# Optimization experiments

Measured on AMD Instinct MI355X. Metric: run time of the kernel, lower is better.

## Reference

```python
import jax, jax.numpy as jnp
import numpy as np

B, N, D = 8, 8192, 512
WS = 128          # ATTENTION_WINDOW_SIZE
LB = 1            # ATTENTION_WINDOW_LOOKBACK (look_backward)
NW = N // WS      # number of windows (N divisible by WS -> autopad no-op)


def setup_inputs() -> dict:
    key = jax.random.key(0)
    ks = jax.random.split(key, 4)
    s = 0.02
    return {
        "x": jax.random.normal(ks[0], (B, N, D), dtype=jnp.float32),
        "w_q": jax.random.normal(ks[1], (D, D), dtype=jnp.float32) * s,
        "b_q": jnp.zeros((D,), dtype=jnp.float32),
        "w_k": jax.random.normal(ks[2], (D, D), dtype=jnp.float32) * s,
        "b_k": jnp.zeros((D,), dtype=jnp.float32),
        "w_v": jax.random.normal(ks[3], (D, D), dtype=jnp.float32) * s,
        "b_v": jnp.zeros((D,), dtype=jnp.float32),
    }


def _look_around(t, pad_value):
    # t: (B, NW, WS, ...) -> concat of [backward..current] windows along window-length axis
    pad_width = [(0, 0), (LB, 0)] + [(0, 0)] * (t.ndim - 2)
    padded = jnp.pad(t, pad_width, constant_values=pad_value)
    return jnp.concatenate([padded[:, i:i + NW] for i in range(LB + 1)], axis=2)


def _local_attention(q, k, v):
    scale = D ** -0.5
    bq = q.reshape(B, NW, WS, D)
    bk = _look_around(k.reshape(B, NW, WS, D), 0.0)   # (B, NW, (LB+1)*WS, D)
    bv = _look_around(v.reshape(B, NW, WS, D), 0.0)

    # absolute position ticks for causal + padding masks
    tq = jnp.arange(N).reshape(1, NW, WS)                               # query positions
    tk = _look_around(jnp.arange(N).reshape(1, NW, WS), -1)             # key positions, -1 = pad

    sim = jnp.einsum('bwie,bwje->bwij', bq, bk) * scale                 # (B, NW, WS, (LB+1)*WS)
    mask = (tq[..., :, None] < tk[..., None, :]) | (tk[..., None, :] < 0)
    sim = jnp.where(mask, -jnp.finfo(sim.dtype).max, sim)
    attn = jax.nn.softmax(sim, axis=-1)                                  # dropout = 0 -> no-op
    out = jnp.einsum('bwij,bwje->bwie', attn, bv)
    return out.reshape(B, N, D)


def reference(x, w_q, b_q, w_k, b_k, w_v, b_v):
    q = x @ w_q.T + b_q
    k = x @ w_k.T + b_k
    v = x @ w_v.T + b_v
    return _local_attention(q, k, v)
```

## Files before the change

### kernel.cpp

```cpp
#include <hip/hip_runtime.h>


typedef __bf16 bf16x8 __attribute__((ext_vector_type(8)));
typedef float f32x4 __attribute__((ext_vector_type(4)));
typedef unsigned short u16x8 __attribute__((ext_vector_type(8)));

#define BATCH 8
#define SEQ   8192
#define DIM   512
#define NWIN  64
#define TOKS  (BATCH * SEQ)
#define WSELEM ((size_t)TOKS * DIM)

__device__ __forceinline__ unsigned short f2b(float f) {
    union { float f; unsigned int u; } c; c.f = f;
    unsigned int u = c.u;
    return (unsigned short)((u + 0x7FFFu + ((u >> 16) & 1u)) >> 16);
}

__device__ __forceinline__ int swz64(int row, int col) {
    return (row * 64 + col) ^ ((row & 7) << 3);
}

__device__ __forceinline__ void gload_lds16(const unsigned short* g,
                                            unsigned short* l) {
    __builtin_amdgcn_global_load_lds(
        (const __attribute__((address_space(1))) void*)g,
        (__attribute__((address_space(3))) void*)l, 16, 0, 0);
}

__global__ __launch_bounds__(256) void k_cvt(const float* __restrict__ s,
                                             unsigned short* __restrict__ d,
                                             int n8) {
    const int stride = gridDim.x * blockDim.x;
    for (int i = blockIdx.x * blockDim.x + threadIdx.x; i < n8; i += stride) {
        const float4 a = ((const float4*)s)[2 * i];
        const float4 b = ((const float4*)s)[2 * i + 1];
        u16x8 v;
        v[0] = f2b(a.x); v[1] = f2b(a.y); v[2] = f2b(a.z); v[3] = f2b(a.w);
        v[4] = f2b(b.x); v[5] = f2b(b.y); v[6] = f2b(b.z); v[7] = f2b(b.w);
        ((u16x8*)d)[i] = v;
    }
}

__global__ __launch_bounds__(256, 2) void k_qkv(
    const unsigned short* __restrict__ xb, const unsigned short* __restrict__ wb,
    const float* __restrict__ bq, const float* __restrict__ bk,
    const float* __restrict__ bv,
    unsigned short* __restrict__ qo, unsigned short* __restrict__ ko,
    unsigned short* __restrict__ vto)
{
    __shared__ __align__(16) unsigned short sm[32768];
    unsigned short* Xs = sm;

    int bid = (int)blockIdx.x;
    bid = (bid & 7) * 256 + (bid >> 3);
    const int mt = bid >> 2, nt = bid & 3;
    const int rbase = mt << 7;
    const int cbase = nt << 7;

    const unsigned short* __restrict__ xsrc0 = xb + ((size_t)rbase << 9);
    const unsigned short* __restrict__ wsrc0 = wb + ((size_t)cbase << 9);

    const int tid  = threadIdx.x;
    const int lane = tid & 63;
    const int wid  = tid >> 6;
    const int wm = wid >> 1, wn = wid & 1;
    const int l15 = lane & 15, lg = lane >> 4;

    f32x4 acc[3][4][4];
#pragma unroll
    for (int s = 0; s < 3; ++s)
#pragma unroll
        for (int m = 0; m < 4; ++m)
#pragma unroll
            for (int n = 0; n < 4; ++n) acc[s][m][n] = (f32x4){0.f, 0.f, 0.f, 0.f};

    const int srow = tid >> 3;
    const int gs   = ((tid & 7) ^ (srow & 7)) << 3;
    const int ldso = tid << 3;

    for (int ks = 0; ks < 8; ++ks) {
        const int kc = ks << 6;
#pragma unroll
        for (int i = 0; i < 4; ++i) {
            const int row = (i << 5) + srow;
            gload_lds16(xsrc0 + ((size_t)row << 9) + kc + gs, Xs + (i << 11) + ldso);
        }
#pragma unroll
        for (int ws = 0; ws < 3; ++ws) {
#pragma unroll
            for (int i = 0; i < 4; ++i) {
                const int row = (i << 5) + srow;
                gload_lds16(wsrc0 + ((size_t)ws << 18) + ((size_t)row << 9) + kc + gs,
                            sm + 8192 + (ws << 13) + (i << 11) + ldso);
            }
        }
        __syncthreads();
#pragma unroll
        for (int kk = 0; kk < 64; kk += 32) {
            const int cu = kk + (lg << 3);
            bf16x8 af[4];
#pragma unroll
            for (int m = 0; m < 4; ++m)
                af[m] = *(const bf16x8*)&Xs[swz64((wm << 6) + (m << 4) + l15, cu)];
#pragma unroll
            for (int ws = 0; ws < 3; ++ws) {
                const unsigned short* Wsb = sm + 8192 + (ws << 13);
                bf16x8 bfr[4];
#pragma unroll
                for (int n = 0; n < 4; ++n)
                    bfr[n] = *(const bf16x8*)&Wsb[swz64((wn << 6) + (n << 4) + l15, cu)];
#pragma unroll
                for (int m = 0; m < 4; ++m)
#pragma unroll
                    for (int n = 0; n < 4; ++n)
                        acc[ws][m][n] = __builtin_amdgcn_mfma_f32_16x16x32_bf16(
                            af[m], bfr[n], acc[ws][m][n], 0, 0, 0);
            }
        }
        __syncthreads();
    }

#pragma unroll
    for (int ws = 0; ws < 2; ++ws) {
        unsigned short* __restrict__ out = ws ? ko : qo;
        const float* __restrict__ bias = ws ? bk : bq;
#pragma unroll
        for (int n = 0; n < 4; ++n) {
            const int col = cbase + (wn << 6) + (n << 4) + l15;
            const float bv_ = bias[col];
#pragma unroll
            for (int m = 0; m < 4; ++m)
#pragma unroll
                for (int j = 0; j < 4; ++j) {
                    const int row = rbase + (wm << 6) + (m << 4) + (lg << 2) + j;
                    out[(size_t)row * DIM + col] = f2b(acc[ws][m][n][j] + bv_);
                }
        }
    }
#pragma unroll
    for (int n = 0; n < 4; ++n) {
        const int dv = (wn << 6) + (n << 4) + l15;
        const float bv_ = bv[cbase + dv];
#pragma unroll
        for (int m = 0; m < 4; ++m)
#pragma unroll
            for (int j = 0; j < 4; ++j) {
                const int tok = (wm << 6) + (m << 4) + (lg << 2) + j;
                sm[tok * 129 + dv] = f2b(acc[2][m][n][j] + bv_);
            }
    }
    __syncthreads();
    {
        const int batch = rbase >> 13;
        const int c5_0  = (rbase & 8191) >> 5;
#pragma unroll
        for (int s = 0; s < 8; ++s) {
            const int c5sel = s & 3, dvh = s >> 2;
            const int dvl  = (dvh << 6) + (wid << 4) + (lane >> 2);
            const int keyo = (lane & 3) << 3;
            const int tok0 = (c5sel << 5) + keyo;
            u16x8 v;
#pragma unroll
            for (int j = 0; j < 8; ++j) v[j] = sm[(tok0 + j) * 129 + dvl];
            *(u16x8*)&vto[((size_t)((batch * 256 + c5_0 + c5sel) * 512
                                    + cbase + dvl) << 5) + keyo] = v;
        }
    }
}

__global__ __launch_bounds__(512, 2) void k_attn(
    const unsigned short* __restrict__ q,
    const unsigned short* __restrict__ k,
    const unsigned short* __restrict__ vt3,
    float* __restrict__ out)
{
    __shared__ __align__(16) unsigned short Kb[32768];
    __shared__ __align__(16) unsigned short Pl[32768];

    int bid = (int)blockIdx.x;
    bid = (bid & 7) * 64 + (bid >> 3);
    const int b = bid >> 6, w = bid & 63;
    const int tid  = threadIdx.x;
    const int lane = tid & 63, wid = tid >> 6;
    const int l15 = lane & 15, lg = lane >> 4;
    const int kstart = (w - 1) << 7;
    const size_t qrow0 = ((size_t)b << 13) + ((size_t)w << 7);
    const size_t kbase = (size_t)b << 13;

    const int srow = tid >> 3;
    const int s0   = tid & 7;

    f32x4 acc[16];
#pragma unroll
    for (int n = 0; n < 16; ++n) acc[n] = (f32x4){0.f, 0.f, 0.f, 0.f};

    auto stageK = [&](int buf, int ds) {
#pragma unroll
        for (int i = 0; i < 4; ++i) {
            const int r = (i << 6) + srow;
            int krow = kstart + r; krow = krow < 0 ? 0 : krow;
            gload_lds16(k + (kbase + krow) * DIM + (ds << 6) + ((s0 ^ (r & 7)) << 3),
                        Kb + (buf << 14) + (i << 12) + (tid << 3));
        }
    };

    stageK(0, 0);
    stageK(1, 1);
    __syncthreads();
    for (int ds = 0; ds < 8; ++ds) {
        const unsigned short* Kc = Kb + ((ds & 1) << 14);
#pragma unroll
        for (int kk2 = 0; kk2 < 2; ++kk2) {
            const int cu = (kk2 << 5) + (lg << 3);
            const bf16x8 af = *(const bf16x8*)
                &q[(qrow0 + (wid << 4) + l15) * DIM + (ds << 6) + cu];
#pragma unroll
            for (int n = 0; n < 16; ++n) {
                const bf16x8 bf = *(const bf16x8*)&Kc[swz64((n << 4) + l15, cu)];
                acc[n] = __builtin_amdgcn_mfma_f32_16x16x32_bf16(af, bf, acc[n], 0, 0, 0);
            }
        }
        __syncthreads();
        if (ds + 2 < 8) stageK(ds & 1, ds + 2);
    }

    const int c5base = kstart >> 5;
    auto stageV = [&](int buf, int kk) {
        int c5 = c5base + kk; c5 = c5 < 0 ? 0 : c5;
        const unsigned short* src = vt3 + ((size_t)(b * 256 + c5) << 14);
#pragma unroll
        for (int i = 0; i < 4; ++i)
            gload_lds16(src + (i << 12) + (tid << 3),
                        Kb + (buf << 14) + (i << 12) + (tid << 3));
    };
    stageV(0, 0);
    stageV(1, 1);

    const float scale = 0.04419417382415922f;
    float inv[4];
    unsigned short* Pw = Pl + (wid << 12);
#pragma unroll
    for (int jj = 0; jj < 4; ++jj) {
        const int r  = (lg << 2) + jj;
        const int qr = (wid << 4) + r;
        float mx = -3.0e38f;
#pragma unroll
        for (int n = 0; n < 16; ++n) {
            const int c = (n << 4) + l15;
            const bool keep = (c <= qr + 128) && (w > 0 || c >= 128);
            const float s = keep ? acc[n][jj] * scale : -INFINITY;
            acc[n][jj] = s;
            mx = fmaxf(mx, s);
        }
#pragma unroll
        for (int o = 1; o < 16; o <<= 1) mx = fmaxf(mx, __shfl_xor(mx, o));
        float sum = 0.f;
#pragma unroll
        for (int n = 0; n < 16; ++n) {
            const float p = __expf(acc[n][jj] - mx);
            acc[n][jj] = p;
            sum += p;
        }
#pragma unroll
        for (int o = 1; o < 16; o <<= 1) sum += __shfl_xor(sum, o);
        inv[jj] = 1.0f / sum;
#pragma unroll
        for (int n = 0; n < 16; ++n) {
            const int c = (n << 4) + l15;
            Pw[(r << 8) + ((((c >> 3) ^ r) << 3) | (c & 7))] = f2b(acc[n][jj]);
        }
    }
    __syncthreads();

    f32x4 oacc[32];
#pragma unroll
    for (int n = 0; n < 32; ++n) oacc[n] = (f32x4){0.f, 0.f, 0.f, 0.f};

    for (int kk = 0; kk < 8; ++kk) {
        const unsigned short* Vc = Kb + ((kk & 1) << 14);
        const bf16x8 pa = *(const bf16x8*)
            &Pw[(l15 << 8) + ((((kk << 2) + lg) ^ l15) << 3)];
#pragma unroll
        for (int n = 0; n < 32; ++n) {
            const bf16x8 bv_ = *(const bf16x8*)&Vc[(((n << 4) + l15) << 5) + (lg << 3)];
            oacc[n] = __builtin_amdgcn_mfma_f32_16x16x32_bf16(pa, bv_, oacc[n], 0, 0, 0);
        }
        if (kk < 7) {
            __syncthreads();
            if (kk + 2 < 8) stageV(kk & 1, kk + 2);
        }
    }

#pragma unroll
    for (int n = 0; n < 32; ++n) {
        const int dv = (n << 4) + l15;
        float* orow = out + (qrow0 + (wid << 4) + (lg << 2)) * DIM + dv;
#pragma unroll
        for (int jj = 0; jj < 4; ++jj)
            orow[(size_t)jj * DIM] = oacc[n][jj] * inv[jj];
    }
}

extern "C" void kernel_launch(void* const* d_in, const int* in_sizes, int n_in,
                              void* d_out, int out_size, void* d_ws, size_t ws_size,
                              hipStream_t stream) {
    (void)in_sizes; (void)n_in; (void)out_size; (void)ws_size;
    const float* x  = (const float*)d_in[0];
    const float* wq = (const float*)d_in[1];
    const float* bq = (const float*)d_in[2];
    const float* wk = (const float*)d_in[3];
    const float* bk = (const float*)d_in[4];
    const float* wv = (const float*)d_in[5];
    const float* bv = (const float*)d_in[6];
    float* out = (float*)d_out;

    unsigned short* qws  = (unsigned short*)d_ws;
    unsigned short* kws  = qws + WSELEM;
    unsigned short* vtws = kws + WSELEM;

    unsigned short* xbuf = (unsigned short*)d_out;
    unsigned short* wbuf = xbuf + WSELEM;

    k_cvt<<<2048, 256, 0, stream>>>(x, xbuf, (int)(WSELEM / 8));
    k_cvt<<<128, 256, 0, stream>>>(wq, wbuf, DIM * DIM / 8);
    k_cvt<<<128, 256, 0, stream>>>(wk, wbuf + DIM * DIM, DIM * DIM / 8);
    k_cvt<<<128, 256, 0, stream>>>(wv, wbuf + 2 * DIM * DIM, DIM * DIM / 8);
    k_qkv<<<2048, 256, 0, stream>>>(xbuf, wbuf, bq, bk, bv, qws, kws, vtws);
    k_attn<<<512, 512, 0, stream>>>(qws, kws, vtws, out);
}
```

Baseline: 242.4 us.

## Double-buffer QKV GEMM with 256-row tiles and 512-thread blocks

The QKV projection kernel now uses 256-row output tiles with 8 waves per block, and half as many blocks. The K loop becomes 16 steps of 32, with two LDS buffers, so the next slice is prefetched by global_load_lds while MFMAs run on the current one. That leaves one barrier per step instead of a load-then-compute pattern with two barriers. The swizzle changes to a 32-column scheme and the V-transpose epilogue is remapped for the larger tile. LDS per block grows to 80 KB, which may limit occupancy, and it relies on enough registers for 2 blocks of 512 threads.

Result: slower. 257.5 us (+6.2%).

```diff
diff --git a/kernel.cpp b/kernel.cpp
--- a/kernel.cpp
+++ b/kernel.cpp
@@ -20,6 +20,9 @@
 
 __device__ __forceinline__ int swz64(int row, int col) {
     return (row * 64 + col) ^ ((row & 7) << 3);
+}
+__device__ __forceinline__ int swz32(int row, int col) {
+    return row * 32 + (col ^ ((row & 3) << 3));
 }
 
 __device__ __forceinline__ void gload_lds16(const unsigned short* g,
@@ -43,20 +46,18 @@
     }
 }
 
-__global__ __launch_bounds__(256, 2) void k_qkv(
+__global__ __launch_bounds__(512, 2) void k_qkv(
     const unsigned short* __restrict__ xb, const unsigned short* __restrict__ wb,
     const float* __restrict__ bq, const float* __restrict__ bk,
     const float* __restrict__ bv,
     unsigned short* __restrict__ qo, unsigned short* __restrict__ ko,
     unsigned short* __restrict__ vto)
 {
-    __shared__ __align__(16) unsigned short sm[32768];
-    unsigned short* Xs = sm;
-
+    __shared__ __align__(16) unsigned short sm[40960];
     int bid = (int)blockIdx.x;
-    bid = (bid & 7) * 256 + (bid >> 3);
+    bid = (bid & 7) * 128 + (bid >> 3);
     const int mt = bid >> 2, nt = bid & 3;
-    const int rbase = mt << 7;
+    const int rbase = mt << 8;
     const int cbase = nt << 7;
 
     const unsigned short* __restrict__ xsrc0 = xb + ((size_t)rbase << 9);
@@ -76,48 +77,49 @@
 #pragma unroll
             for (int n = 0; n < 4; ++n) acc[s][m][n] = (f32x4){0.f, 0.f, 0.f, 0.f};
 
-    const int srow = tid >> 3;
-    const int gs   = ((tid & 7) ^ (srow & 7)) << 3;
-    const int ldso = tid << 3;
-
-    for (int ks = 0; ks < 8; ++ks) {
-        const int kc = ks << 6;
-#pragma unroll
-        for (int i = 0; i < 4; ++i) {
-            const int row = (i << 5) + srow;
-            gload_lds16(xsrc0 + ((size_t)row << 9) + kc + gs, Xs + (i << 11) + ldso);
+    const int tr = tid >> 2;
+    const int sl = tid & 3;
+
+    auto stage = [&](int b, int ks) {
+        const int kc = ks << 5;
+        unsigned short* Xb = sm + b * 20480;
+#pragma unroll
+        for (int i = 0; i < 2; ++i) {
+            const int r = (i << 7) + tr;
+            gload_lds16(xsrc0 + ((size_t)r << 9) + kc + ((sl ^ (r & 3)) << 3),
+                        Xb + (i << 12) + (tid << 3));
         }
 #pragma unroll
         for (int ws = 0; ws < 3; ++ws) {
-#pragma unroll
-            for (int i = 0; i < 4; ++i) {
-                const int row = (i << 5) + srow;
-                gload_lds16(wsrc0 + ((size_t)ws << 18) + ((size_t)row << 9) + kc + gs,
-                            sm + 8192 + (ws << 13) + (i << 11) + ldso);
-            }
-        }
-        __syncthreads();
-#pragma unroll
-        for (int kk = 0; kk < 64; kk += 32) {
-            const int cu = kk + (lg << 3);
-            bf16x8 af[4];
+            gload_lds16(wsrc0 + ((size_t)ws << 18) + ((size_t)(tr & 127) << 9)
+                            + kc + ((sl ^ (tr & 3)) << 3),
+                        Xb + 8192 + (ws << 12) + (tid << 3));
+        }
+    };
+
+    stage(0, 0);
+    __syncthreads();
+    for (int ks = 0; ks < 16; ++ks) {
+        if (ks < 15) stage((ks + 1) & 1, ks + 1);
+        const unsigned short* Xb = sm + (ks & 1) * 20480;
+        const int cu = lg << 3;
+        bf16x8 af[4];
+#pragma unroll
+        for (int m = 0; m < 4; ++m)
+            af[m] = *(const bf16x8*)&Xb[swz32((wm << 6) + (m << 4) + l15, cu)];
+#pragma unroll
+        for (int ws = 0; ws < 3; ++ws) {
+            const unsigned short* Wsb = Xb + 8192 + (ws << 12);
+            bf16x8 bfr[4];
+#pragma unroll
+            for (int n = 0; n < 4; ++n)
+                bfr[n] = *(const bf16x8*)&Wsb[swz32((wn << 6) + (n << 4) + l15, cu)];
 #pragma unroll
             for (int m = 0; m < 4; ++m)
-                af[m] = *(const bf16x8*)&Xs[swz64((wm << 6) + (m << 4) + l15, cu)];
-#pragma unroll
-            for (int ws = 0; ws < 3; ++ws) {
-                const unsigned short* Wsb = sm + 8192 + (ws << 13);
-                bf16x8 bfr[4];
 #pragma unroll
                 for (int n = 0; n < 4; ++n)
-                    bfr[n] = *(const bf16x8*)&Wsb[swz64((wn << 6) + (n << 4) + l15, cu)];
-#pragma unroll
-                for (int m = 0; m < 4; ++m)
-#pragma unroll
-                    for (int n = 0; n < 4; ++n)
-                        acc[ws][m][n] = __builtin_amdgcn_mfma_f32_16x16x32_bf16(
-                            af[m], bfr[n], acc[ws][m][n], 0, 0, 0);
-            }
+                    acc[ws][m][n] = __builtin_amdgcn_mfma_f32_16x16x32_bf16(
+                        af[m], bfr[n], acc[ws][m][n], 0, 0, 0);
         }
         __syncthreads();
     }
@@ -155,16 +157,15 @@
     {
         const int batch = rbase >> 13;
         const int c5_0  = (rbase & 8191) >> 5;
+        const int dvl   = tid >> 2;
+        const int keyo  = (tid & 3) << 3;
 #pragma unroll
         for (int s = 0; s < 8; ++s) {
-            const int c5sel = s & 3, dvh = s >> 2;
-            const int dvl  = (dvh << 6) + (wid << 4) + (lane >> 2);
-            const int keyo = (lane & 3) << 3;
-            const int tok0 = (c5sel << 5) + keyo;
+            const int tok0 = (s << 5) + keyo;
             u16x8 v;
 #pragma unroll
             for (int j = 0; j < 8; ++j) v[j] = sm[(tok0 + j) * 129 + dvl];
-            *(u16x8*)&vto[((size_t)((batch * 256 + c5_0 + c5sel) * 512
+            *(u16x8*)&vto[((size_t)((batch * 256 + c5_0 + s) * 512
                                     + cbase + dvl) << 5) + keyo] = v;
         }
     }
@@ -327,6 +328,6 @@
     k_cvt<<<128, 256, 0, stream>>>(wq, wbuf, DIM * DIM / 8);
     k_cvt<<<128, 256, 0, stream>>>(wk, wbuf + DIM * DIM, DIM * DIM / 8);
     k_cvt<<<128, 256, 0, stream>>>(wv, wbuf + 2 * DIM * DIM, DIM * DIM / 8);
-    k_qkv<<<2048, 256, 0, stream>>>(xbuf, wbuf, bq, bk, bv, qws, kws, vtws);
+    k_qkv<<<1024, 512, 0, stream>>>(xbuf, wbuf, bq, bk, bv, qws, kws, vtws);
     k_attn<<<512, 512, 0, stream>>>(qws, kws, vtws, out);
 }
```

## Restructure QKV GEMM into 128x256 tiles with triple-buffered async LDS pipeline

Applied to the files above, without the earlier changes.

The QKV projection kernel now has each 512-thread block compute one 128x256 output tile of a single projection (Q, K or V), instead of a 128x128 tile across all three. The K loop is software-pipelined with a three-stage LDS ring: loads for stage t+2 are issued before stage t's MFMAs, with vmcnt waits and raw s_barrier in place of full __syncthreads. The goal is to hide global-to-LDS latency and cut per-block accumulator pressure. The cost is more LDS per block (144KB) and more blocks, which may limit occupancy, and the V transpose path is rewritten with a wider LDS stride.

Measured after the change: 260.2 us. 1.07x slower.

```diff
diff --git a/kernel.cpp b/kernel.cpp
--- a/kernel.cpp
+++ b/kernel.cpp
@@ -28,6 +28,8 @@
         (const __attribute__((address_space(1))) void*)g,
         (__attribute__((address_space(3))) void*)l, 16, 0, 0);
 }
+
+#define VMCNT(n) asm volatile("s_waitcnt vmcnt(" #n ")" ::: "memory")
 
 __global__ __launch_bounds__(256) void k_cvt(const float* __restrict__ s,
                                              unsigned short* __restrict__ d,
@@ -43,129 +45,131 @@
     }
 }
 
-__global__ __launch_bounds__(256, 2) void k_qkv(
+__global__ __launch_bounds__(512, 2) void k_qkv(
     const unsigned short* __restrict__ xb, const unsigned short* __restrict__ wb,
     const float* __restrict__ bq, const float* __restrict__ bk,
     const float* __restrict__ bv,
     unsigned short* __restrict__ qo, unsigned short* __restrict__ ko,
     unsigned short* __restrict__ vto)
 {
-    __shared__ __align__(16) unsigned short sm[32768];
-    unsigned short* Xs = sm;
-
+    __shared__ __align__(16) unsigned short sm[73728];
     int bid = (int)blockIdx.x;
-    bid = (bid & 7) * 256 + (bid >> 3);
-    const int mt = bid >> 2, nt = bid & 3;
+    bid = (bid & 7) * 384 + (bid >> 3);
+    const int mt = bid / 6, nt = bid - mt * 6;
     const int rbase = mt << 7;
-    const int cbase = nt << 7;
+    const int op  = nt >> 1;
+    const int cop = (nt & 1) << 8;
 
     const unsigned short* __restrict__ xsrc0 = xb + ((size_t)rbase << 9);
-    const unsigned short* __restrict__ wsrc0 = wb + ((size_t)cbase << 9);
+    const unsigned short* __restrict__ bsrc0 = wb + ((size_t)nt << 17);
 
     const int tid  = threadIdx.x;
     const int lane = tid & 63;
     const int wid  = tid >> 6;
-    const int wm = wid >> 1, wn = wid & 1;
+    const int wm = wid >> 2, wn = wid & 3;
     const int l15 = lane & 15, lg = lane >> 4;
 
-    f32x4 acc[3][4][4];
-#pragma unroll
-    for (int s = 0; s < 3; ++s)
-#pragma unroll
-        for (int m = 0; m < 4; ++m)
-#pragma unroll
-            for (int n = 0; n < 4; ++n) acc[s][m][n] = (f32x4){0.f, 0.f, 0.f, 0.f};
-
-    const int srow = tid >> 3;
-    const int gs   = ((tid & 7) ^ (srow & 7)) << 3;
-    const int ldso = tid << 3;
-
-    for (int ks = 0; ks < 8; ++ks) {
-        const int kc = ks << 6;
+    f32x4 acc[4][4];
+#pragma unroll
+    for (int m = 0; m < 4; ++m)
+#pragma unroll
+        for (int n = 0; n < 4; ++n) acc[m][n] = (f32x4){0.f, 0.f, 0.f, 0.f};
+
+    const int r0 = tid >> 3;
+    const int sl = tid & 7;
+
+    auto stage = [&](int t) {
+        unsigned short* buf = sm + (t % 3) * 24576;
+        const int kc = t << 6;
+#pragma unroll
+        for (int i = 0; i < 2; ++i) {
+            const int r = (i << 6) + r0;
+            gload_lds16(xsrc0 + ((size_t)r << 9) + kc + ((sl ^ (r & 7)) << 3),
+                        buf + (i << 12) + (tid << 3));
+        }
 #pragma unroll
         for (int i = 0; i < 4; ++i) {
-            const int row = (i << 5) + srow;
-            gload_lds16(xsrc0 + ((size_t)row << 9) + kc + gs, Xs + (i << 11) + ldso);
-        }
-#pragma unroll
-        for (int ws = 0; ws < 3; ++ws) {
-#pragma unroll
-            for (int i = 0; i < 4; ++i) {
-                const int row = (i << 5) + srow;
-                gload_lds16(wsrc0 + ((size_t)ws << 18) + ((size_t)row << 9) + kc + gs,
-                            sm + 8192 + (ws << 13) + (i << 11) + ldso);
-            }
-        }
-        __syncthreads();
-#pragma unroll
-        for (int kk = 0; kk < 64; kk += 32) {
-            const int cu = kk + (lg << 3);
-            bf16x8 af[4];
+            const int r = (i << 6) + r0;
+            gload_lds16(bsrc0 + ((size_t)r << 9) + kc + ((sl ^ (r & 7)) << 3),
+                        buf + 8192 + (i << 12) + (tid << 3));
+        }
+    };
+
+    stage(0);
+    stage(1);
+    VMCNT(6);
+    __builtin_amdgcn_s_barrier();
+
+#pragma unroll
+    for (int t = 0; t < 8; ++t) {
+        if (t < 6) stage(t + 2);
+        const unsigned short* Ab = sm + (t % 3) * 24576;
+        const unsigned short* Bb = Ab + 8192;
+#pragma unroll
+        for (int kk = 0; kk < 2; ++kk) {
+            const int cu = (kk << 5) + (lg << 3);
+            bf16x8 af[4], bfr[4];
 #pragma unroll
             for (int m = 0; m < 4; ++m)
-                af[m] = *(const bf16x8*)&Xs[swz64((wm << 6) + (m << 4) + l15, cu)];
-#pragma unroll
-            for (int ws = 0; ws < 3; ++ws) {
-                const unsigned short* Wsb = sm + 8192 + (ws << 13);
-                bf16x8 bfr[4];
+                af[m] = *(const bf16x8*)&Ab[swz64((wm << 6) + (m << 4) + l15, cu)];
+#pragma unroll
+            for (int n = 0; n < 4; ++n)
+                bfr[n] = *(const bf16x8*)&Bb[swz64((wn << 6) + (n << 4) + l15, cu)];
+#pragma unroll
+            for (int m = 0; m < 4; ++m)
 #pragma unroll
                 for (int n = 0; n < 4; ++n)
-                    bfr[n] = *(const bf16x8*)&Wsb[swz64((wn << 6) + (n << 4) + l15, cu)];
-#pragma unroll
-                for (int m = 0; m < 4; ++m)
-#pragma unroll
-                    for (int n = 0; n < 4; ++n)
-                        acc[ws][m][n] = __builtin_amdgcn_mfma_f32_16x16x32_bf16(
-                            af[m], bfr[n], acc[ws][m][n], 0, 0, 0);
-            }
-        }
-        __syncthreads();
-    }
-
-#pragma unroll
-    for (int ws = 0; ws < 2; ++ws) {
-        unsigned short* __restrict__ out = ws ? ko : qo;
-        const float* __restrict__ bias = ws ? bk : bq;
+                    acc[m][n] = __builtin_amdgcn_mfma_f32_16x16x32_bf16(
+                        af[m], bfr[n], acc[m][n], 0, 0, 0);
+        }
+        if (t < 6) { VMCNT(6); }
+        else if (t == 6) { VMCNT(0); }
+        if (t < 7) __builtin_amdgcn_s_barrier();
+    }
+
+    if (op < 2) {
+        unsigned short* __restrict__ out = op ? ko : qo;
+        const float* __restrict__ bias = op ? bk : bq;
 #pragma unroll
         for (int n = 0; n < 4; ++n) {
-            const int col = cbase + (wn << 6) + (n << 4) + l15;
+            const int col = cop + (wn << 6) + (n << 4) + l15;
             const float bv_ = bias[col];
 #pragma unroll
             for (int m = 0; m < 4; ++m)
 #pragma unroll
                 for (int j = 0; j < 4; ++j) {
                     const int row = rbase + (wm << 6) + (m << 4) + (lg << 2) + j;
-                    out[(size_t)row * DIM + col] = f2b(acc[ws][m][n][j] + bv_);
+                    out[(size_t)row * DIM + col] = f2b(acc[m][n][j] + bv_);
                 }
         }
-    }
-#pragma unroll
-    for (int n = 0; n < 4; ++n) {
-        const int dv = (wn << 6) + (n << 4) + l15;
-        const float bv_ = bv[cbase + dv];
-#pragma unroll
-        for (int m = 0; m < 4; ++m)
-#pragma unroll
-            for (int j = 0; j < 4; ++j) {
-                const int tok = (wm << 6) + (m << 4) + (lg << 2) + j;
-                sm[tok * 129 + dv] = f2b(acc[2][m][n][j] + bv_);
-            }
-    }
-    __syncthreads();
-    {
+    } else {
+        __syncthreads();
+#pragma unroll
+        for (int n = 0; n < 4; ++n) {
+            const int dvl = (wn << 6) + (n << 4) + l15;
+            const float bv_ = bv[cop + dvl];
+#pragma unroll
+            for (int m = 0; m < 4; ++m)
+#pragma unroll
+                for (int j = 0; j < 4; ++j) {
+                    const int tok = (wm << 6) + (m << 4) + (lg << 2) + j;
+                    sm[tok * 264 + dvl] = f2b(acc[m][n][j] + bv_);
+                }
+        }
+        __syncthreads();
         const int batch = rbase >> 13;
         const int c5_0  = (rbase & 8191) >> 5;
+        const int keyo  = (tid & 3) << 3;
 #pragma unroll
         for (int s = 0; s < 8; ++s) {
-            const int c5sel = s & 3, dvh = s >> 2;
-            const int dvl  = (dvh << 6) + (wid << 4) + (lane >> 2);
-            const int keyo = (lane & 3) << 3;
+            const int c5sel = s & 3, h = s >> 2;
+            const int dvl  = (h << 7) + (tid >> 2);
             const int tok0 = (c5sel << 5) + keyo;
             u16x8 v;
 #pragma unroll
-            for (int j = 0; j < 8; ++j) v[j] = sm[(tok0 + j) * 129 + dvl];
+            for (int j = 0; j < 8; ++j) v[j] = sm[(tok0 + j) * 264 + dvl];
             *(u16x8*)&vto[((size_t)((batch * 256 + c5_0 + c5sel) * 512
-                                    + cbase + dvl) << 5) + keyo] = v;
+                                    + cop + dvl) << 5) + keyo] = v;
         }
     }
 }
@@ -327,6 +331,6 @@
     k_cvt<<<128, 256, 0, stream>>>(wq, wbuf, DIM * DIM / 8);
     k_cvt<<<128, 256, 0, stream>>>(wk, wbuf + DIM * DIM, DIM * DIM / 8);
     k_cvt<<<128, 256, 0, stream>>>(wv, wbuf + 2 * DIM * DIM, DIM * DIM / 8);
-    k_qkv<<<2048, 256, 0, stream>>>(xbuf, wbuf, bq, bk, bv, qws, kws, vtws);
+    k_qkv<<<3072, 512, 0, stream>>>(xbuf, wbuf, bq, bk, bv, qws, kws, vtws);
     k_attn<<<512, 512, 0, stream>>>(qws, kws, vtws, out);
 }
```

## Halve QKV GEMM K-tile to 32 with paired-row LDS swizzle

Applied to the files above, without the earlier changes.

The QKV projection GEMM now stages 32-wide K slices instead of 64-wide ones, taking 16 iterations instead of 8. This halves the shared-memory footprint (about 33 KB instead of 64 KB). A new swizzle packs two 32-element rows into each 64-element LDS line, aiming to keep reads free of bank conflicts. The occupancy hint of 2 blocks per SM is dropped from launch bounds, which may let more blocks fit thanks to the smaller LDS use. The trade-off is twice as many barriers and global-to-LDS load rounds, with no overlap between loading and MFMA work.

Measured after the change: 338.6 us. 1.4x slower.

```diff
diff --git a/kernel.cpp b/kernel.cpp
--- a/kernel.cpp
+++ b/kernel.cpp
@@ -20,6 +20,12 @@
 
 __device__ __forceinline__ int swz64(int row, int col) {
     return (row * 64 + col) ^ ((row & 7) << 3);
+}
+
+__device__ __forceinline__ int swzp(int row, int cu) {
+    const int p = row >> 1;
+    const int q = (((row & 1) << 2) | (cu >> 3)) ^ (p & 7);
+    return p * 64 + q * 8;
 }
 
 __device__ __forceinline__ void gload_lds16(const unsigned short* g,
@@ -43,16 +49,14 @@
     }
 }
 
-__global__ __launch_bounds__(256, 2) void k_qkv(
+__global__ __launch_bounds__(256) void k_qkv(
     const unsigned short* __restrict__ xb, const unsigned short* __restrict__ wb,
     const float* __restrict__ bq, const float* __restrict__ bk,
     const float* __restrict__ bv,
     unsigned short* __restrict__ qo, unsigned short* __restrict__ ko,
     unsigned short* __restrict__ vto)
 {
-    __shared__ __align__(16) unsigned short sm[32768];
-    unsigned short* Xs = sm;
-
+    __shared__ __align__(16) unsigned short sm[16512];
     int bid = (int)blockIdx.x;
     bid = (bid & 7) * 256 + (bid >> 3);
     const int mt = bid >> 2, nt = bid & 3;
@@ -76,41 +80,42 @@
 #pragma unroll
             for (int n = 0; n < 4; ++n) acc[s][m][n] = (f32x4){0.f, 0.f, 0.f, 0.f};
 
-    const int srow = tid >> 3;
-    const int gs   = ((tid & 7) ^ (srow & 7)) << 3;
-    const int ldso = tid << 3;
-
-    for (int ks = 0; ks < 8; ++ks) {
-        const int kc = ks << 6;
-#pragma unroll
-        for (int i = 0; i < 4; ++i) {
-            const int row = (i << 5) + srow;
-            gload_lds16(xsrc0 + ((size_t)row << 9) + kc + gs, Xs + (i << 11) + ldso);
-        }
-#pragma unroll
-        for (int ws = 0; ws < 3; ++ws) {
-#pragma unroll
-            for (int i = 0; i < 4; ++i) {
-                const int row = (i << 5) + srow;
-                gload_lds16(wsrc0 + ((size_t)ws << 18) + ((size_t)row << 9) + kc + gs,
-                            sm + 8192 + (ws << 13) + (i << 11) + ldso);
-            }
+    int srow[2], scol[2];
+#pragma unroll
+    for (int i = 0; i < 2; ++i) {
+        const int s = (i << 8) + tid;
+        const int p = s >> 3;
+        const int e = (s & 7) ^ (p & 7);
+        srow[i] = (p << 1) + (e >> 2);
+        scol[i] = (e & 3) << 3;
+    }
+
+    for (int ks = 0; ks < 16; ++ks) {
+        const int kc = ks << 5;
+#pragma unroll
+        for (int i = 0; i < 2; ++i) {
+            const int dst = ((i << 8) + tid) << 3;
+            gload_lds16(xsrc0 + ((size_t)srow[i] << 9) + kc + scol[i], sm + dst);
+#pragma unroll
+            for (int ws = 0; ws < 3; ++ws)
+                gload_lds16(wsrc0 + ((size_t)ws << 18) + ((size_t)srow[i] << 9)
+                                + kc + scol[i],
+                            sm + 4096 + (ws << 12) + dst);
         }
         __syncthreads();
-#pragma unroll
-        for (int kk = 0; kk < 64; kk += 32) {
-            const int cu = kk + (lg << 3);
+        {
+            const int cu = lg << 3;
             bf16x8 af[4];
 #pragma unroll
             for (int m = 0; m < 4; ++m)
-                af[m] = *(const bf16x8*)&Xs[swz64((wm << 6) + (m << 4) + l15, cu)];
+                af[m] = *(const bf16x8*)&sm[swzp((wm << 6) + (m << 4) + l15, cu)];
 #pragma unroll
             for (int ws = 0; ws < 3; ++ws) {
-                const unsigned short* Wsb = sm + 8192 + (ws << 13);
+                const unsigned short* Wsb = sm + 4096 + (ws << 12);
                 bf16x8 bfr[4];
 #pragma unroll
                 for (int n = 0; n < 4; ++n)
-                    bfr[n] = *(const bf16x8*)&Wsb[swz64((wn << 6) + (n << 4) + l15, cu)];
+                    bfr[n] = *(const bf16x8*)&Wsb[swzp((wn << 6) + (n << 4) + l15, cu)];
 #pragma unroll
                 for (int m = 0; m < 4; ++m)
 #pragma unroll
```
